# Performance work log

Measured on AMD Instinct MI355X. Metric: run time of the kernel, lower is better.

The kernel has to match this reference:

```python
import jax, jax.numpy as jnp
import numpy as np

FDIM = 128
NHEADS = 4
HDIM = FDIM // NHEADS
SIGMA2 = 2.0 * 0.3 ** 2


def _layernorm(h, w, b):
    m = h.mean(-1, keepdims=True)
    v = ((h - m) ** 2).mean(-1, keepdims=True)
    return (h - m) / jnp.sqrt(v + 1e-5) * w + b


def setup_inputs() -> dict:
    key = jax.random.key(0)
    ks = jax.random.split(key, 10)
    B, C, H, W = 16, FDIM, 128, 128
    Hm, Wm = 1024, 1024
    inp = {
        'x': jax.random.normal(ks[0], (B, C, H, W), jnp.float32),
        'masks': jax.random.uniform(ks[1], (B, 2, Hm, Wm), jnp.float32),
        'Wq': jax.random.normal(ks[2], (FDIM, FDIM), jnp.float32) * 0.02,
        'bq': jnp.zeros((FDIM,), jnp.float32),
        'Wk': jax.random.normal(ks[3], (FDIM, FDIM), jnp.float32) * 0.02,
        'bk': jnp.zeros((FDIM,), jnp.float32),
        'Wv': jax.random.normal(ks[4], (FDIM, FDIM), jnp.float32) * 0.02,
        'bv': jnp.zeros((FDIM,), jnp.float32),
        'Wo': jax.random.normal(ks[5], (FDIM, FDIM), jnp.float32) * 0.02,
        'bo': jnp.zeros((FDIM,), jnp.float32),
        'ln1_w': jnp.ones((FDIM,), jnp.float32),
        'ln1_b': jnp.zeros((FDIM,), jnp.float32),
        'W1': jax.random.normal(ks[6], (2 * FDIM, FDIM), jnp.float32) * 0.02,
        'b1': jnp.zeros((2 * FDIM,), jnp.float32),
        'W2': jax.random.normal(ks[7], (FDIM, 2 * FDIM), jnp.float32) * 0.02,
        'b2': jnp.zeros((FDIM,), jnp.float32),
        'ln2_w': jnp.ones((FDIM,), jnp.float32),
        'ln2_b': jnp.zeros((FDIM,), jnp.float32),
    }
    return inp


def reference(x, masks, Wq, bq, Wk, bk, Wv, bv, Wo, bo, ln1_w, ln1_b, W1, b1, W2, b2, ln2_w, ln2_b):
    B, C, H, W = x.shape
    Hm, Wm = masks.shape[2], masks.shape[3]
    # nearest-neighbor downsample of masks to feature-map size (torch 'nearest')
    iy = jnp.arange(H) * Hm // H
    ix = jnp.arange(W) * Wm // W
    m = masks[:, :, iy][:, :, :, ix]                      # (B, 2, H, W), raw values
    binm = (m > 0.5).astype(x.dtype)                       # thresholded for centroids

    # --- node pooling (vectorized extract_nodes_from_masks; both masks nonempty) ---
    nodes0 = jnp.einsum('bchw,bnhw->bnc', x, m) / (m.sum((2, 3))[..., None] + 1e-6)
    cnt = jnp.maximum(binm.sum((2, 3)), 1.0)               # (B, 2)
    ys = jnp.arange(H, dtype=x.dtype)
    xs = jnp.arange(W, dtype=x.dtype)
    cy = jnp.einsum('bnhw,h->bn', binm, ys) / cnt
    cx = jnp.einsum('bnhw,w->bn', binm, xs) / cnt
    pos = jnp.stack([cx / W * 2 - 1, cy / H * 2 - 1], -1)  # (B, N, 2) = (pos_x, pos_y)

    # --- distance-biased multi-head graph attention ---
    B_, N, _ = nodes0.shape
    def proj(t, Wp, bp):
        return (t @ Wp.T + bp).reshape(B_, N, NHEADS, HDIM).transpose(0, 2, 1, 3)
    Q = proj(nodes0, Wq, bq)
    K = proj(nodes0, Wk, bk)
    V = proj(nodes0, Wv, bv)
    scores = jnp.einsum('bhnd,bhmd->bhnm', Q, K) / (HDIM ** 0.5)
    d2 = jnp.sum((pos[:, :, None] - pos[:, None, :]) ** 2, -1)
    dist = jnp.where(d2 > 0, jnp.sqrt(jnp.where(d2 > 0, d2, 1.0)), 0.0)  # safe cdist
    attn = jax.nn.softmax(scores - dist[:, None], axis=-1)
    out = jnp.einsum('bhnm,bhmd->bhnd', attn, V).transpose(0, 2, 1, 3).reshape(B_, N, C)
    out = out @ Wo.T + bo
    nodes = _layernorm(nodes0 + out, ln1_w, ln1_b)
    ffn = jax.nn.relu(nodes @ W1.T + b1) @ W2.T + b2
    nodes = _layernorm(nodes + ffn, ln2_w, ln2_b)        # (B, N, C)

    # --- Gaussian broadcast of nodes back to the feature map ---
    yg = jnp.linspace(-1.0, 1.0, H)
    xg = jnp.linspace(-1.0, 1.0, W)
    dx = xg[None, None, None, :] - pos[:, :, 0][:, :, None, None]  # (B,N,1,W)
    dy = yg[None, None, :, None] - pos[:, :, 1][:, :, None, None]  # (B,N,H,1)
    wgt = jnp.exp(-(dx ** 2 + dy ** 2) / SIGMA2)                   # (B,N,H,W)
    graph_features = jnp.einsum('bnc,bnhw->bchw', nodes, wgt)
    return x + graph_features
```

## Files before the change

kernel.cpp:

```cpp
#include <hip/hip_runtime.h>
#include <cstdint>
#include <cstddef>

#define NB 16
#define NC 128
#define NH 128
#define NW 128
#define HM 1024
#define WM 1024
#define HW (NH*NW)
#define NHEADS 4
#define HDIM 32
#define INV_SIGMA2 5.555555555555555f

#define WS_M     0
#define WS_PART  524288
#define WS_NUM   525312
#define WS_NODES 529408
#define WS_WXY   533504

__device__ __forceinline__ float dot4(float4 a, float4 b) {
    return a.x*b.x + a.y*b.y + a.z*b.z + a.w*b.w;
}

__global__ void kA(const float* __restrict__ masks, float* __restrict__ ws) {
    float* m_ds = ws + WS_M;
    float* part = ws + WS_PART;
    int blk = blockIdx.x;
    int b2 = blk >> 3;
    int chunk = blk & 7;
    int tid = threadIdx.x;
    int wcol = tid & 127;
    int rofs = tid >> 7;
    const float* mp = masks + (size_t)b2 * (HM * WM);
    float msum = 0.f, cnt = 0.f, cy = 0.f, cx = 0.f;
#pragma unroll
    for (int it = 0; it < 8; ++it) {
        int r = chunk * 16 + it * 2 + rofs;
        float v = mp[(size_t)(r * 8) * WM + wcol * 8];
        m_ds[(size_t)b2 * HW + r * 128 + wcol] = v;
        msum += v;
        if (v > 0.5f) { cnt += 1.0f; cy += (float)r; cx += (float)wcol; }
    }
    __shared__ float wred[4][4];
#pragma unroll
    for (int s = 32; s > 0; s >>= 1) {
        msum += __shfl_down(msum, s, 64);
        cnt  += __shfl_down(cnt,  s, 64);
        cy   += __shfl_down(cy,   s, 64);
        cx   += __shfl_down(cx,   s, 64);
    }
    if ((tid & 63) == 0) {
        int w = tid >> 6;
        wred[w][0] = msum; wred[w][1] = cnt; wred[w][2] = cy; wred[w][3] = cx;
    }
    __syncthreads();
    if (tid == 0) {
        float* p = part + (b2 * 8 + chunk) * 4;
        p[0] = wred[0][0] + wred[1][0] + wred[2][0] + wred[3][0];
        p[1] = wred[0][1] + wred[1][1] + wred[2][1] + wred[3][1];
        p[2] = wred[0][2] + wred[1][2] + wred[2][2] + wred[3][2];
        p[3] = wred[0][3] + wred[1][3] + wred[2][3] + wred[3][3];
    }
}

__global__ void kB(const float* __restrict__ x, const float* __restrict__ ws_full) {
    const float* ws_m = ws_full + WS_M;
    float* num = (float*)(ws_full + WS_NUM);
    int b = blockIdx.x >> 7, c = blockIdx.x & 127;
    int tid = threadIdx.x;
    const float4* xp = (const float4*)(x + ((size_t)b * NC + c) * HW);
    const float4* m0 = (const float4*)(ws_m + (size_t)(b * 2 + 0) * HW);
    const float4* m1 = (const float4*)(ws_m + (size_t)(b * 2 + 1) * HW);
    float a0 = 0.f, a1 = 0.f;
#pragma unroll
    for (int i = 0; i < 16; ++i) {
        int idx = i * 256 + tid;
        float4 xv = xp[idx];
        float4 v0 = m0[idx];
        float4 v1 = m1[idx];
        a0 += xv.x*v0.x + xv.y*v0.y + xv.z*v0.z + xv.w*v0.w;
        a1 += xv.x*v1.x + xv.y*v1.y + xv.z*v1.z + xv.w*v1.w;
    }
    __shared__ float wred[4][2];
#pragma unroll
    for (int s = 32; s > 0; s >>= 1) {
        a0 += __shfl_down(a0, s, 64);
        a1 += __shfl_down(a1, s, 64);
    }
    if ((tid & 63) == 0) { wred[tid >> 6][0] = a0; wred[tid >> 6][1] = a1; }
    __syncthreads();
    if (tid == 0) {
        num[(b * 2 + 0) * 128 + c] = wred[0][0] + wred[1][0] + wred[2][0] + wred[3][0];
        num[(b * 2 + 1) * 128 + c] = wred[0][1] + wred[1][1] + wred[2][1] + wred[3][1];
    }
}

__global__ void kC(const float* __restrict__ Wq, const float* __restrict__ bq,
                   const float* __restrict__ Wk, const float* __restrict__ bk,
                   const float* __restrict__ Wv, const float* __restrict__ bv,
                   const float* __restrict__ Wo, const float* __restrict__ bo,
                   const float* __restrict__ ln1w, const float* __restrict__ ln1b,
                   const float* __restrict__ W1, const float* __restrict__ b1,
                   const float* __restrict__ W2, const float* __restrict__ b2,
                   const float* __restrict__ ln2w, const float* __restrict__ ln2b,
                   float* __restrict__ ws) {
    int b = blockIdx.x;
    int tid = threadIdx.x;
    int c = tid & 127;
    int i = tid >> 7;

    const float* part = ws + WS_PART;
    const float* num  = ws + WS_NUM;
    float* nodesf = ws + WS_NODES;
    float* wxy    = ws + WS_WXY;

    __shared__ __align__(16) float s_n0[2][128];
    __shared__ __align__(16) float sQ[2][128], sK[2][128], sV[2][128];
    __shared__ __align__(16) float s_o[2][128];
    __shared__ __align__(16) float s_h1[2][128];
    __shared__ __align__(16) float s_n1[2][128];
    __shared__ __align__(16) float s_hid[2][256];
    __shared__ __align__(16) float s_h2[2][128];
    __shared__ float red[4];
    __shared__ float s_sc[16];
    __shared__ float s_at[NHEADS][2][2];
    __shared__ float s_px[2], s_py[2], s_den[2];

    if (tid < 2) {
        int n = tid;
        float msum = 0.f, cnt = 0.f, cy = 0.f, cx = 0.f;
        const float* p = part + ((b * 2 + n) * 8) * 4;
        for (int ch = 0; ch < 8; ++ch) {
            msum += p[ch*4+0]; cnt += p[ch*4+1]; cy += p[ch*4+2]; cx += p[ch*4+3];
        }
        s_den[n] = msum + 1e-6f;
        float cm = fmaxf(cnt, 1.0f);
        s_px[n] = (cx / cm) / 64.0f - 1.0f;
        s_py[n] = (cy / cm) / 64.0f - 1.0f;
    }
    __syncthreads();

    s_n0[i][c] = num[(b * 2 + i) * 128 + c] / s_den[i];
    __syncthreads();

    {
        float4 na0 = ((const float4*)s_n0[0])[tid & 31];
        float4 na1 = ((const float4*)s_n0[1])[tid & 31];
        const float4* Wq4 = (const float4*)Wq;
        const float4* Wk4 = (const float4*)Wk;
        const float4* Wv4 = (const float4*)Wv;
#pragma unroll 4
        for (int p = 0; p < 16; ++p) {
            int e4 = p * 256 + tid;
            float4 wq = Wq4[e4], wk = Wk4[e4], wv = Wv4[e4];
            int cc = e4 >> 5;
            float q0 = dot4(wq, na0), q1 = dot4(wq, na1);
            float k0v = dot4(wk, na0), k1v = dot4(wk, na1);
            float v0 = dot4(wv, na0), v1 = dot4(wv, na1);
#pragma unroll
            for (int s = 16; s > 0; s >>= 1) {
                q0  += __shfl_down(q0,  s, 32); q1  += __shfl_down(q1,  s, 32);
                k0v += __shfl_down(k0v, s, 32); k1v += __shfl_down(k1v, s, 32);
                v0  += __shfl_down(v0,  s, 32); v1  += __shfl_down(v1,  s, 32);
            }
            if ((tid & 31) == 0) {
                float bQ = bq[cc], bK = bk[cc], bV = bv[cc];
                sQ[0][cc] = q0 + bQ;  sQ[1][cc] = q1 + bQ;
                sK[0][cc] = k0v + bK; sK[1][cc] = k1v + bK;
                sV[0][cc] = v0 + bV;  sV[1][cc] = v1 + bV;
            }
        }
    }
    __syncthreads();

    if (tid < 16) {
        int h = tid >> 2, ii = (tid >> 1) & 1, j = tid & 1;
        float s = 0.f;
        for (int d = 0; d < HDIM; ++d) s += sQ[ii][h*HDIM+d] * sK[j][h*HDIM+d];
        s *= 0.17677669529663687f;
        if (ii != j) {
            float dx = s_px[0] - s_px[1], dy = s_py[0] - s_py[1];
            float d2 = dx*dx + dy*dy;
            if (d2 > 0.f) s -= sqrtf(d2);
        }
        s_sc[tid] = s;
    }
    __syncthreads();

    if (tid < 8) {
        int h = tid >> 1, ii = tid & 1;
        float s0 = s_sc[h*4 + ii*2 + 0], s1 = s_sc[h*4 + ii*2 + 1];
        float mx = fmaxf(s0, s1);
        float e0 = expf(s0 - mx), e1 = expf(s1 - mx);
        float inv = 1.0f / (e0 + e1);
        s_at[h][ii][0] = e0 * inv;
        s_at[h][ii][1] = e1 * inv;
    }
    __syncthreads();

    {
        int h = c >> 5;
        s_o[i][c] = s_at[h][i][0] * sV[0][c] + s_at[h][i][1] * sV[1][c];
    }
    __syncthreads();

    {
        float4 oa0 = ((const float4*)s_o[0])[tid & 31];
        float4 oa1 = ((const float4*)s_o[1])[tid & 31];
        const float4* Wo4 = (const float4*)Wo;
#pragma unroll 4
        for (int p = 0; p < 16; ++p) {
            int e4 = p * 256 + tid;
            float4 w = Wo4[e4];
            int cc = e4 >> 5;
            float v0 = dot4(w, oa0), v1 = dot4(w, oa1);
#pragma unroll
            for (int s = 16; s > 0; s >>= 1) {
                v0 += __shfl_down(v0, s, 32); v1 += __shfl_down(v1, s, 32);
            }
            if ((tid & 31) == 0) {
                float bb = bo[cc];
                s_h1[0][cc] = v0 + bb + s_n0[0][cc];
                s_h1[1][cc] = v1 + bb + s_n0[1][cc];
            }
        }
    }
    __syncthreads();

    {
        float h = s_h1[i][c];
        float v = h;
#pragma unroll
        for (int s = 32; s > 0; s >>= 1) v += __shfl_down(v, s, 64);
        if ((tid & 63) == 0) red[tid >> 6] = v;
        __syncthreads();
        float mean = (red[i*2] + red[i*2+1]) * (1.0f / 128.0f);
        float d = h - mean;
        float v2 = d * d;
        __syncthreads();
#pragma unroll
        for (int s = 32; s > 0; s >>= 1) v2 += __shfl_down(v2, s, 64);
        if ((tid & 63) == 0) red[tid >> 6] = v2;
        __syncthreads();
        float var = (red[i*2] + red[i*2+1]) * (1.0f / 128.0f);
        s_n1[i][c] = d * rsqrtf(var + 1e-5f) * ln1w[c] + ln1b[c];
    }
    __syncthreads();

    {
        float4 na0 = ((const float4*)s_n1[0])[tid & 31];
        float4 na1 = ((const float4*)s_n1[1])[tid & 31];
        const float4* W1_4 = (const float4*)W1;
#pragma unroll 4
        for (int p = 0; p < 32; ++p) {
            int e4 = p * 256 + tid;
            float4 w = W1_4[e4];
            int j = e4 >> 5;
            float v0 = dot4(w, na0), v1 = dot4(w, na1);
#pragma unroll
            for (int s = 16; s > 0; s >>= 1) {
                v0 += __shfl_down(v0, s, 32); v1 += __shfl_down(v1, s, 32);
            }
            if ((tid & 31) == 0) {
                float bb = b1[j];
                s_hid[0][j] = fmaxf(v0 + bb, 0.0f);
                s_hid[1][j] = fmaxf(v1 + bb, 0.0f);
            }
        }
    }
    __syncthreads();

    {
        float4 ha0 = ((const float4*)s_hid[0])[tid & 63];
        float4 ha1 = ((const float4*)s_hid[1])[tid & 63];
        const float4* W2_4 = (const float4*)W2;
#pragma unroll 4
        for (int p = 0; p < 32; ++p) {
            int e4 = p * 256 + tid;
            float4 w = W2_4[e4];
            int cc = e4 >> 6;
            float v0 = dot4(w, ha0), v1 = dot4(w, ha1);
#pragma unroll
            for (int s = 32; s > 0; s >>= 1) {
                v0 += __shfl_down(v0, s, 64); v1 += __shfl_down(v1, s, 64);
            }
            if ((tid & 63) == 0) {
                float bb = b2[cc];
                s_h2[0][cc] = v0 + bb + s_n1[0][cc];
                s_h2[1][cc] = v1 + bb + s_n1[1][cc];
            }
        }
    }
    __syncthreads();

    {
        float h = s_h2[i][c];
        float v = h;
#pragma unroll
        for (int s = 32; s > 0; s >>= 1) v += __shfl_down(v, s, 64);
        if ((tid & 63) == 0) red[tid >> 6] = v;
        __syncthreads();
        float mean = (red[i*2] + red[i*2+1]) * (1.0f / 128.0f);
        float d = h - mean;
        float v2 = d * d;
        __syncthreads();
#pragma unroll
        for (int s = 32; s > 0; s >>= 1) v2 += __shfl_down(v2, s, 64);
        if ((tid & 63) == 0) red[tid >> 6] = v2;
        __syncthreads();
        float var = (red[i*2] + red[i*2+1]) * (1.0f / 128.0f);
        nodesf[(b * 2 + i) * 128 + c] = d * rsqrtf(var + 1e-5f) * ln2w[c] + ln2b[c];
    }

    {
        float g = (float)c * (2.0f / 127.0f) - 1.0f;
        float dx = g - s_px[i];
        float dy = g - s_py[i];
        wxy[((b*2+i)*2 + 0) * 128 + c] = expf(-dx * dx * INV_SIGMA2);
        wxy[((b*2+i)*2 + 1) * 128 + c] = expf(-dy * dy * INV_SIGMA2);
    }
}

__global__ void kD(const float* __restrict__ x, const float* __restrict__ ws,
                   float* __restrict__ out) {
    const float* nodesf = ws + WS_NODES;
    const float* wxy    = ws + WS_WXY;
    int b = blockIdx.x >> 7, c = blockIdx.x & 127;
    int tid = threadIdx.x;
    __shared__ float4 swx0[32], swx1[32];
    __shared__ float swy0[128], swy1[128];
    if (tid < 128) {
        swy0[tid] = wxy[((b*2+0)*2 + 1) * 128 + tid];
        swy1[tid] = wxy[((b*2+1)*2 + 1) * 128 + tid];
    } else {
        int t = tid - 128;
        if (t < 32)      swx0[t]      = ((const float4*)(wxy + ((b*2+0)*2 + 0) * 128))[t];
        else if (t < 64) swx1[t - 32] = ((const float4*)(wxy + ((b*2+1)*2 + 0) * 128))[t - 32];
    }
    float n0 = nodesf[(b * 2 + 0) * 128 + c];
    float n1 = nodesf[(b * 2 + 1) * 128 + c];
    __syncthreads();
    const float4* xp = (const float4*)(x   + ((size_t)b * NC + c) * HW);
    float4*       op = (float4*)      (out + ((size_t)b * NC + c) * HW);
#pragma unroll
    for (int it = 0; it < 16; ++it) {
        int p4 = it * 256 + tid;
        int h = p4 >> 5;
        int w4 = p4 & 31;
        float a0 = n0 * swy0[h];
        float a1 = n1 * swy1[h];
        float4 xv = xp[p4];
        float4 wx0 = swx0[w4], wx1 = swx1[w4];
        float4 r;
        r.x = xv.x + a0 * wx0.x + a1 * wx1.x;
        r.y = xv.y + a0 * wx0.y + a1 * wx1.y;
        r.z = xv.z + a0 * wx0.z + a1 * wx1.z;
        r.w = xv.w + a0 * wx0.w + a1 * wx1.w;
        op[p4] = r;
    }
}

extern "C" void kernel_launch(void* const* d_in, const int* in_sizes, int n_in,
                              void* d_out, int out_size, void* d_ws, size_t ws_size,
                              hipStream_t stream) {
    const float* x     = (const float*)d_in[0];
    const float* masks = (const float*)d_in[1];
    const float* Wq    = (const float*)d_in[2];
    const float* bq    = (const float*)d_in[3];
    const float* Wk    = (const float*)d_in[4];
    const float* bk    = (const float*)d_in[5];
    const float* Wv    = (const float*)d_in[6];
    const float* bv    = (const float*)d_in[7];
    const float* Wo    = (const float*)d_in[8];
    const float* bo    = (const float*)d_in[9];
    const float* ln1w  = (const float*)d_in[10];
    const float* ln1b  = (const float*)d_in[11];
    const float* W1    = (const float*)d_in[12];
    const float* b1    = (const float*)d_in[13];
    const float* W2    = (const float*)d_in[14];
    const float* b2    = (const float*)d_in[15];
    const float* ln2w  = (const float*)d_in[16];
    const float* ln2b  = (const float*)d_in[17];
    float* out = (float*)d_out;
    float* ws  = (float*)d_ws;

    hipLaunchKernelGGL(kA, dim3(NB * 2 * 8), dim3(256), 0, stream, masks, ws);
    hipLaunchKernelGGL(kB, dim3(NB * NC), dim3(256), 0, stream, x, ws);
    hipLaunchKernelGGL(kC, dim3(NB), dim3(256), 0, stream,
                       Wq, bq, Wk, bk, Wv, bv, Wo, bo, ln1w, ln1b,
                       W1, b1, W2, b2, ln2w, ln2b, ws);
    hipLaunchKernelGGL(kD, dim3(NB * NC), dim3(256), 0, stream, x, ws, out);
}
```

Baseline: 423.4 us.

## Restructure node MLP kernel to per-thread row dot products with register-prefetched weights

The small per-batch attention/FFN kernel now gives each thread (or thread pair) a whole weight row instead of striding across rows with wide shuffle reductions. Weight rows for Q/K/V, Wo, W1 and W2 are loaded into registers early so later loads overlap earlier compute, and bias/layernorm parameters are hoisted. This removes most cross-lane shuffle reductions and serialized global-load latency, at the cost of very high register use (launch_bounds 256,1), uncoalesced row-wise loads, and possible spills.

```diff
diff --git a/kernel.cpp b/kernel.cpp
--- a/kernel.cpp
+++ b/kernel.cpp
@@ -96,19 +96,22 @@
     }
 }
 
-__global__ void kC(const float* __restrict__ Wq, const float* __restrict__ bq,
-                   const float* __restrict__ Wk, const float* __restrict__ bk,
-                   const float* __restrict__ Wv, const float* __restrict__ bv,
-                   const float* __restrict__ Wo, const float* __restrict__ bo,
-                   const float* __restrict__ ln1w, const float* __restrict__ ln1b,
-                   const float* __restrict__ W1, const float* __restrict__ b1,
-                   const float* __restrict__ W2, const float* __restrict__ b2,
-                   const float* __restrict__ ln2w, const float* __restrict__ ln2b,
-                   float* __restrict__ ws) {
+__global__ void __launch_bounds__(256, 1)
+kC(const float* __restrict__ Wq, const float* __restrict__ bq,
+   const float* __restrict__ Wk, const float* __restrict__ bk,
+   const float* __restrict__ Wv, const float* __restrict__ bv,
+   const float* __restrict__ Wo, const float* __restrict__ bo,
+   const float* __restrict__ ln1w, const float* __restrict__ ln1b,
+   const float* __restrict__ W1, const float* __restrict__ b1,
+   const float* __restrict__ W2, const float* __restrict__ b2,
+   const float* __restrict__ ln2w, const float* __restrict__ ln2b,
+   float* __restrict__ ws) {
     int b = blockIdx.x;
     int tid = threadIdx.x;
     int c = tid & 127;
     int i = tid >> 7;
+    int r = tid >> 1;
+    int hv = tid & 1;
 
     const float* part = ws + WS_PART;
     const float* num  = ws + WS_NUM;
@@ -127,6 +130,21 @@
     __shared__ float s_at[NHEADS][2][2];
     __shared__ float s_px[2], s_py[2], s_den[2];
 
+    const float4* Wq4 = (const float4*)Wq + (r << 5) + (hv << 4);
+    const float4* Wk4 = (const float4*)Wk + (r << 5) + (hv << 4);
+    const float4* Wv4 = (const float4*)Wv + (r << 5) + (hv << 4);
+    float4 wq[16], wk[16], wv[16];
+#pragma unroll
+    for (int k = 0; k < 16; ++k) wq[k] = Wq4[k];
+#pragma unroll
+    for (int k = 0; k < 16; ++k) wk[k] = Wk4[k];
+#pragma unroll
+    for (int k = 0; k < 16; ++k) wv[k] = Wv4[k];
+    float biasq = bq[r], biask = bk[r], biasv = bv[r], biaso = bo[r];
+    float bias1 = b1[tid];
+    float bias2 = b2[r];
+    float l1w = ln1w[c], l1b = ln1b[c], l2w = ln2w[c], l2b = ln2b[c];
+
     if (tid < 2) {
         int n = tid;
         float msum = 0.f, cnt = 0.f, cy = 0.f, cx = 0.f;
@@ -145,33 +163,35 @@
     __syncthreads();
 
     {
-        float4 na0 = ((const float4*)s_n0[0])[tid & 31];
-        float4 na1 = ((const float4*)s_n0[1])[tid & 31];
-        const float4* Wq4 = (const float4*)Wq;
-        const float4* Wk4 = (const float4*)Wk;
-        const float4* Wv4 = (const float4*)Wv;
-#pragma unroll 4
-        for (int p = 0; p < 16; ++p) {
-            int e4 = p * 256 + tid;
-            float4 wq = Wq4[e4], wk = Wk4[e4], wv = Wv4[e4];
-            int cc = e4 >> 5;
-            float q0 = dot4(wq, na0), q1 = dot4(wq, na1);
-            float k0v = dot4(wk, na0), k1v = dot4(wk, na1);
-            float v0 = dot4(wv, na0), v1 = dot4(wv, na1);
-#pragma unroll
-            for (int s = 16; s > 0; s >>= 1) {
-                q0  += __shfl_down(q0,  s, 32); q1  += __shfl_down(q1,  s, 32);
-                k0v += __shfl_down(k0v, s, 32); k1v += __shfl_down(k1v, s, 32);
-                v0  += __shfl_down(v0,  s, 32); v1  += __shfl_down(v1,  s, 32);
-            }
-            if ((tid & 31) == 0) {
-                float bQ = bq[cc], bK = bk[cc], bV = bv[cc];
-                sQ[0][cc] = q0 + bQ;  sQ[1][cc] = q1 + bQ;
-                sK[0][cc] = k0v + bK; sK[1][cc] = k1v + bK;
-                sV[0][cc] = v0 + bV;  sV[1][cc] = v1 + bV;
-            }
-        }
-    }
+        const float4* a0 = (const float4*)&s_n0[0][0] + (hv << 4);
+        const float4* a1 = (const float4*)&s_n0[1][0] + (hv << 4);
+        float q0 = 0.f, q1 = 0.f, k0v = 0.f, k1v = 0.f, v0 = 0.f, v1 = 0.f;
+#pragma unroll
+        for (int k = 0; k < 16; ++k) {
+            float4 x0 = a0[k], x1 = a1[k];
+            q0  += dot4(wq[k], x0); q1  += dot4(wq[k], x1);
+            k0v += dot4(wk[k], x0); k1v += dot4(wk[k], x1);
+            v0  += dot4(wv[k], x0); v1  += dot4(wv[k], x1);
+        }
+        q0  += __shfl_xor(q0,  1); q1  += __shfl_xor(q1,  1);
+        k0v += __shfl_xor(k0v, 1); k1v += __shfl_xor(k1v, 1);
+        v0  += __shfl_xor(v0,  1); v1  += __shfl_xor(v1,  1);
+        if (hv == 0) {
+            sQ[0][r] = q0 + biasq;  sQ[1][r] = q1 + biasq;
+            sK[0][r] = k0v + biask; sK[1][r] = k1v + biask;
+            sV[0][r] = v0 + biasv;  sV[1][r] = v1 + biasv;
+        }
+    }
+
+    const float4* Wo4 = (const float4*)Wo + (r << 5) + (hv << 4);
+    float4 wo[16];
+#pragma unroll
+    for (int k = 0; k < 16; ++k) wo[k] = Wo4[k];
+    const float4* W1_4 = (const float4*)W1 + (tid << 5);
+    float4 w1[32];
+#pragma unroll
+    for (int k = 0; k < 32; ++k) w1[k] = W1_4[k];
+
     __syncthreads();
 
     if (tid < 16) {
@@ -206,24 +226,19 @@
     __syncthreads();
 
     {
-        float4 oa0 = ((const float4*)s_o[0])[tid & 31];
-        float4 oa1 = ((const float4*)s_o[1])[tid & 31];
-        const float4* Wo4 = (const float4*)Wo;
-#pragma unroll 4
-        for (int p = 0; p < 16; ++p) {
-            int e4 = p * 256 + tid;
-            float4 w = Wo4[e4];
-            int cc = e4 >> 5;
-            float v0 = dot4(w, oa0), v1 = dot4(w, oa1);
-#pragma unroll
-            for (int s = 16; s > 0; s >>= 1) {
-                v0 += __shfl_down(v0, s, 32); v1 += __shfl_down(v1, s, 32);
-            }
-            if ((tid & 31) == 0) {
-                float bb = bo[cc];
-                s_h1[0][cc] = v0 + bb + s_n0[0][cc];
-                s_h1[1][cc] = v1 + bb + s_n0[1][cc];
-            }
+        const float4* a0 = (const float4*)&s_o[0][0] + (hv << 4);
+        const float4* a1 = (const float4*)&s_o[1][0] + (hv << 4);
+        float v0 = 0.f, v1 = 0.f;
+#pragma unroll
+        for (int k = 0; k < 16; ++k) {
+            v0 += dot4(wo[k], a0[k]);
+            v1 += dot4(wo[k], a1[k]);
+        }
+        v0 += __shfl_xor(v0, 1);
+        v1 += __shfl_xor(v1, 1);
+        if (hv == 0) {
+            s_h1[0][r] = v0 + biaso + s_n0[0][r];
+            s_h1[1][r] = v1 + biaso + s_n0[1][r];
         }
     }
     __syncthreads();
@@ -244,52 +259,44 @@
         if ((tid & 63) == 0) red[tid >> 6] = v2;
         __syncthreads();
         float var = (red[i*2] + red[i*2+1]) * (1.0f / 128.0f);
-        s_n1[i][c] = d * rsqrtf(var + 1e-5f) * ln1w[c] + ln1b[c];
-    }
-    __syncthreads();
-
-    {
-        float4 na0 = ((const float4*)s_n1[0])[tid & 31];
-        float4 na1 = ((const float4*)s_n1[1])[tid & 31];
-        const float4* W1_4 = (const float4*)W1;
-#pragma unroll 4
-        for (int p = 0; p < 32; ++p) {
-            int e4 = p * 256 + tid;
-            float4 w = W1_4[e4];
-            int j = e4 >> 5;
-            float v0 = dot4(w, na0), v1 = dot4(w, na1);
-#pragma unroll
-            for (int s = 16; s > 0; s >>= 1) {
-                v0 += __shfl_down(v0, s, 32); v1 += __shfl_down(v1, s, 32);
-            }
-            if ((tid & 31) == 0) {
-                float bb = b1[j];
-                s_hid[0][j] = fmaxf(v0 + bb, 0.0f);
-                s_hid[1][j] = fmaxf(v1 + bb, 0.0f);
-            }
-        }
-    }
-    __syncthreads();
-
-    {
-        float4 ha0 = ((const float4*)s_hid[0])[tid & 63];
-        float4 ha1 = ((const float4*)s_hid[1])[tid & 63];
-        const float4* W2_4 = (const float4*)W2;
-#pragma unroll 4
-        for (int p = 0; p < 32; ++p) {
-            int e4 = p * 256 + tid;
-            float4 w = W2_4[e4];
-            int cc = e4 >> 6;
-            float v0 = dot4(w, ha0), v1 = dot4(w, ha1);
-#pragma unroll
-            for (int s = 32; s > 0; s >>= 1) {
-                v0 += __shfl_down(v0, s, 64); v1 += __shfl_down(v1, s, 64);
-            }
-            if ((tid & 63) == 0) {
-                float bb = b2[cc];
-                s_h2[0][cc] = v0 + bb + s_n1[0][cc];
-                s_h2[1][cc] = v1 + bb + s_n1[1][cc];
-            }
+        s_n1[i][c] = d * rsqrtf(var + 1e-5f) * l1w + l1b;
+    }
+    __syncthreads();
+
+    {
+        const float4* a0 = (const float4*)&s_n1[0][0];
+        const float4* a1 = (const float4*)&s_n1[1][0];
+        float v0 = 0.f, v1 = 0.f;
+#pragma unroll
+        for (int k = 0; k < 32; ++k) {
+            v0 += dot4(w1[k], a0[k]);
+            v1 += dot4(w1[k], a1[k]);
+        }
+        s_hid[0][tid] = fmaxf(v0 + bias1, 0.0f);
+        s_hid[1][tid] = fmaxf(v1 + bias1, 0.0f);
+    }
+
+    const float4* W2_4 = (const float4*)W2 + (r << 6) + (hv << 5);
+    float4 w2[32];
+#pragma unroll
+    for (int k = 0; k < 32; ++k) w2[k] = W2_4[k];
+
+    __syncthreads();
+
+    {
+        const float4* a0 = (const float4*)&s_hid[0][0] + (hv << 5);
+        const float4* a1 = (const float4*)&s_hid[1][0] + (hv << 5);
+        float v0 = 0.f, v1 = 0.f;
+#pragma unroll
+        for (int k = 0; k < 32; ++k) {
+            v0 += dot4(w2[k], a0[k]);
+            v1 += dot4(w2[k], a1[k]);
+        }
+        v0 += __shfl_xor(v0, 1);
+        v1 += __shfl_xor(v1, 1);
+        if (hv == 0) {
+            s_h2[0][r] = v0 + bias2 + s_n1[0][r];
+            s_h2[1][r] = v1 + bias2 + s_n1[1][r];
         }
     }
     __syncthreads();
@@ -310,7 +317,7 @@
         if ((tid & 63) == 0) red[tid >> 6] = v2;
         __syncthreads();
         float var = (red[i*2] + red[i*2+1]) * (1.0f / 128.0f);
-        nodesf[(b * 2 + i) * 128 + c] = d * rsqrtf(var + 1e-5f) * ln2w[c] + ln2b[c];
+        nodesf[(b * 2 + i) * 128 + c] = d * rsqrtf(var + 1e-5f) * l2w + l2b;
     }
 
     {
```

After: 364.3 us. 1.16x faster.
